# Kernel tuning notes

Measured on AMD Instinct MI355X. Metric: run time of the kernel, lower is better.

## Reference

```python
import jax, jax.numpy as jnp
import numpy as np

BN_EPS = 1e-3
NUM_HEADS = 4
HEAD_CH = 16  # embed_channels // num_heads = 64 // 4


def _conv_bn(x, w, g, b, rm, rv, pad):
    # Conv2d (no bias) followed by eval-mode BatchNorm2d, activation=Identity.
    y = jax.lax.conv_general_dilated(
        x, w, window_strides=(1, 1), padding=[(pad, pad), (pad, pad)],
        dimension_numbers=("NCHW", "OIHW", "NCHW"))
    s = g * jax.lax.rsqrt(rv + BN_EPS)
    return y * s[None, :, None, None] + (b - rm * s)[None, :, None, None]


def setup_inputs() -> dict:
    key = jax.random.key(0)
    ks = jax.random.split(key, 16)
    B, Cin, H, W = 8, 128, 160, 160
    N, Cg, Ce, Co = 80, 512, 64, 128
    x = jax.random.normal(ks[0], (B, Cin, H, W), jnp.float32)
    guide = jax.random.normal(ks[1], (B, N, Cg), jnp.float32)
    # embed_conv (1x1) + BN params
    w_embed = jax.random.normal(ks[2], (Ce, Cin, 1, 1), jnp.float32) * 0.05
    g1 = jnp.ones((Ce,), jnp.float32)
    b1 = jnp.zeros((Ce,), jnp.float32)
    rm1 = jax.random.normal(ks[3], (Ce,), jnp.float32) * 0.1
    rv1 = jax.random.uniform(ks[4], (Ce,), jnp.float32) + 0.5
    # guide_fc
    Wg = jax.random.normal(ks[5], (Ce, Cg), jnp.float32) * 0.02
    bg = jnp.zeros((Ce,), jnp.float32)
    # per-head bias
    attn_bias = jnp.zeros((NUM_HEADS,), jnp.float32)
    # project_conv (3x3) + BN params
    w_proj = jax.random.normal(ks[6], (Co, Cin, 3, 3), jnp.float32) * 0.02
    g2 = jnp.ones((Co,), jnp.float32)
    b2 = jnp.zeros((Co,), jnp.float32)
    rm2 = jax.random.normal(ks[7], (Co,), jnp.float32) * 0.1
    rv2 = jax.random.uniform(ks[8], (Co,), jnp.float32) + 0.5
    return {"x": x, "guide": guide, "w_embed": w_embed, "g1": g1, "b1": b1,
            "rm1": rm1, "rv1": rv1, "Wg": Wg, "bg": bg, "attn_bias": attn_bias,
            "w_proj": w_proj, "g2": g2, "b2": b2, "rm2": rm2, "rv2": rv2}


def reference(x, guide, w_embed, g1, b1, rm1, rv1, Wg, bg, attn_bias,
              w_proj, g2, b2, rm2, rv2):
    B, _, H, W = x.shape
    nh, hc = NUM_HEADS, HEAD_CH
    # guide_fc -> [B, N, nh, hc]
    g = (jnp.einsum("bnc,ec->bne", guide, Wg) + bg).reshape(B, -1, nh, hc)
    # embed_conv (1x1, BN, no act) -> [B, nh, hc, H, W]
    e = _conv_bn(x, w_embed, g1, b1, rm1, rv1, 0).reshape(B, nh, hc, H, W)
    # attn: dot over head channels, max over N guides, scale, bias, sigmoid
    aw = jnp.einsum("bmchw,bnmc->bmhwn", e, g)  # [B, nh, H, W, N]
    aw = jnp.max(aw, axis=-1) * (1.0 / np.sqrt(hc)) + attn_bias[None, :, None, None]
    aw = jax.nn.sigmoid(aw)  # scale == 1.0 (with_scale=False)
    # project_conv (3x3, BN, no act), gate per-head, merge heads
    xp = _conv_bn(x, w_proj, g2, b2, rm2, rv2, 1).reshape(B, nh, -1, H, W)
    return (xp * aw[:, :, None]).reshape(B, -1, H, W)
```

## Files before the change

### kernel.cpp

```cpp
#include <hip/hip_runtime.h>
#include <hip/hip_bf16.h>
#include <stdint.h>


typedef __attribute__((ext_vector_type(8))) short short8;
typedef __attribute__((ext_vector_type(4))) float f32x4;

#define PCH2 ((size_t)8 * 162 * 176 * 32)

__device__ __forceinline__ unsigned short f2bf(float f) {
  unsigned int u = __float_as_uint(f);
  u += 0x7fff + ((u >> 16) & 1);
  return (unsigned short)(u >> 16);
}

__device__ __forceinline__ short8 zero8() {
  short8 z = {0,0,0,0,0,0,0,0};
  return z;
}

__global__ __launch_bounds__(192) void k_prep_x(const float* __restrict__ x,
                                                unsigned short* __restrict__ P2) {
  int b = blockIdx.x / 162, hp = blockIdx.x % 162;
  int wp = threadIdx.x;
  if (wp >= 176) return;
  size_t pix = (((size_t)b * 162 + hp) * 176 + wp) * 32;
  bool interior = (hp >= 1) && (hp <= 160) && (wp >= 8) && (wp < 168);
  if (!interior) {
#pragma unroll
    for (int cs = 0; cs < 4; ++cs)
#pragma unroll
      for (int s = 0; s < 4; ++s)
        *(short8*)(&P2[(size_t)cs * PCH2 + pix + s * 8]) = zero8();
    return;
  }
  int h = hp - 1, w = wp - 8;
  const float* xb = x + (size_t)b * 128 * 25600 + h * 160 + w;
  for (int cs = 0; cs < 4; ++cs) {
#pragma unroll
    for (int s = 0; s < 4; ++s) {
      short8 v;
#pragma unroll
      for (int j = 0; j < 8; ++j) {
        float f = xb[(size_t)(cs * 32 + s * 8 + j) * 25600];
        v[j] = (short)f2bf(f);
      }
      *(short8*)(&P2[(size_t)cs * PCH2 + pix + s * 8]) = v;
    }
  }
}

__global__ __launch_bounds__(256) void k_prep_misc(
    const float* __restrict__ w_embed, const float* __restrict__ w_proj,
    const float* __restrict__ g2, const float* __restrict__ b2,
    const float* __restrict__ rm2, const float* __restrict__ rv2,
    unsigned short* __restrict__ W1t, unsigned short* __restrict__ Wpt,
    float* __restrict__ s2, float* __restrict__ t2) {
  int idx = blockIdx.x * 256 + threadIdx.x;
  if (idx < 8192) { W1t[idx] = f2bf(w_embed[idx]); return; }
  idx -= 8192;
  if (idx < 147456) {
    int cs = idx / 36864, r = idx - cs * 36864;
    int tap = r >> 12, r2 = r & 4095;
    int co = r2 >> 5, ci5 = r2 & 31;
    int ci = cs * 32 + ci5;
    Wpt[idx] = f2bf(w_proj[(co * 128 + ci) * 9 + tap]);
    return;
  }
  idx -= 147456;
  if (idx < 128) {
    float s = g2[idx] * rsqrtf(rv2[idx] + 1e-3f);
    s2[idx] = s;
    t2[idx] = b2[idx] - rm2[idx] * s;
  }
}

__global__ __launch_bounds__(64) void k_guide(
    const float* __restrict__ guide, const float* __restrict__ Wg,
    const float* __restrict__ bg, const float* __restrict__ g1,
    const float* __restrict__ b1, const float* __restrict__ rm1,
    const float* __restrict__ rv1, unsigned short* __restrict__ Gpad,
    float* __restrict__ Cst) {
  int b = blockIdx.x / 80, n = blockIdx.x % 80;
  __shared__ float gs[512];
  const float* gr = guide + ((size_t)b * 80 + n) * 512;
  for (int i = threadIdx.x; i < 512; i += 64) gs[i] = gr[i];
  __syncthreads();
  int ce = threadIdx.x;
  const float* wr = Wg + (size_t)ce * 512;
  float acc = 0.f;
  for (int k = 0; k < 512; k += 4)
    acc += gs[k] * wr[k] + gs[k + 1] * wr[k + 1] + gs[k + 2] * wr[k + 2] +
           gs[k + 3] * wr[k + 3];
  float raw = acc + bg[ce];
  float s1 = g1[ce] * rsqrtf(rv1[ce] + 1e-3f);
  float t1 = b1[ce] - rm1[ce] * s1;
  int head = ce >> 4, c = ce & 15;
  size_t gp = (((size_t)b * 4 + head) * 80 + n) * 32;
  Gpad[gp + c] = f2bf(raw * s1);
  Gpad[gp + 16 + c] = 0;
  float cp = raw * t1;
  cp += __shfl_xor(cp, 1);
  cp += __shfl_xor(cp, 2);
  cp += __shfl_xor(cp, 4);
  cp += __shfl_xor(cp, 8);
  if (c == 0) Cst[((size_t)b * 4 + head) * 80 + n] = cp;
}

__global__ __launch_bounds__(256, 2) void k_mega(
    const unsigned short* __restrict__ P2, const unsigned short* __restrict__ W1t,
    const unsigned short* __restrict__ Wpt, const unsigned short* __restrict__ Gpad,
    const float* __restrict__ Cst, const float* __restrict__ attn_bias,
    const float* __restrict__ s2, const float* __restrict__ t2,
    float* __restrict__ out) {
  __shared__ unsigned short XA[2][7680];
  __shared__ float AWL[4][2][64];
  int b = blockIdx.x & 7, r2b = blockIdx.x >> 3;
  int ht = r2b / 5, wt = r2b % 5;
  int h0 = ht * 4, w0 = wt * 32;
  int tid = threadIdx.x, lane = tid & 63, wv = tid >> 6;
  int l15 = lane & 15, l4 = lane >> 4;
  int mh = wv >> 1, nh = wv & 1;

  size_t aoff[4];
  bool aval[4];
#pragma unroll
  for (int i = 0; i < 4; ++i) {
    int c = i * 256 + tid;
    aval[i] = (c < 960);
    int cc = aval[i] ? c : 0;
    int row = cc / 160, rem = cc - row * 160;
    int px = rem >> 2, sp = rem & 3;
    int s = sp ^ ((px >> 1) & 3);
    aoff[i] = (((size_t)b * 162 + h0 + row) * 176 + (w0 + 7 + px)) * 32 + s * 8;
  }
  int abase[2][3];
#pragma unroll
  for (int wh = 0; wh < 2; ++wh)
#pragma unroll
    for (int kx = 0; kx < 3; ++kx) {
      int px = wh * 16 + l15 + kx;
      abase[wh][kx] = px * 4 + (l4 ^ ((px >> 1) & 3));
    }
  int bfo = (nh * 64 + l15 * 1 * 16 % 16, 0);
  int bco = (nh * 64 + l15) * 0;
  int boff[4];
#pragma unroll
  for (int nt = 0; nt < 4; ++nt) boff[nt] = (nh * 64 + nt * 16 + l15) * 32 + l4 * 8;

  f32x4 acc[4][4], accE[4][2];
#pragma unroll
  for (int j = 0; j < 4; ++j) {
#pragma unroll
    for (int nt = 0; nt < 4; ++nt) acc[j][nt] = (f32x4){0.f, 0.f, 0.f, 0.f};
#pragma unroll
    for (int ne = 0; ne < 2; ++ne) accE[j][ne] = (f32x4){0.f, 0.f, 0.f, 0.f};
  }

  short8 areg[4];
#pragma unroll
  for (int i = 0; i < 4; ++i)
    if (aval[i]) areg[i] = *(const short8*)(P2 + aoff[i]);
#pragma unroll
  for (int i = 0; i < 4; ++i)
    if (aval[i]) *(short8*)(&XA[0][(i * 256 + tid) * 8]) = areg[i];

  short8 Bbuf[3][4];
#pragma unroll
  for (int nt = 0; nt < 4; ++nt) {
    Bbuf[0][nt] = *(const short8*)(Wpt + boff[nt]);
    Bbuf[1][nt] = *(const short8*)(Wpt + 4096 + boff[nt]);
  }
  __syncthreads();

#pragma unroll
  for (int cs = 0; cs < 4; ++cs) {
    if (cs < 3) {
#pragma unroll
      for (int i = 0; i < 4; ++i)
        if (aval[i]) areg[i] = *(const short8*)(P2 + (size_t)(cs + 1) * PCH2 + aoff[i]);
    }
#pragma unroll
    for (int tap = 0; tap < 9; ++tap) {
      const int t = cs * 9 + tap;
      if (t + 2 < 36) {
#pragma unroll
        for (int nt = 0; nt < 4; ++nt)
          Bbuf[(t + 2) % 3][nt] =
              *(const short8*)(Wpt + (size_t)(t + 2) * 4096 + boff[nt]);
      }
      int ky = tap / 3, kx = tap - ky * 3;
      short8 A[4];
#pragma unroll
      for (int j = 0; j < 4; ++j) {
        int rr = mh * 2 + (j >> 1) + ky;
        A[j] = *(const short8*)(&XA[cs & 1][(rr * 160 + abase[j & 1][kx]) * 8]);
      }
      if (tap == 4) {
        short8 BE[2];
#pragma unroll
        for (int ne = 0; ne < 2; ++ne)
          BE[ne] = *(const short8*)(W1t + (nh * 32 + ne * 16 + l15) * 128 +
                                    cs * 32 + l4 * 8);
#pragma unroll
        for (int j = 0; j < 4; ++j)
#pragma unroll
          for (int ne = 0; ne < 2; ++ne)
            accE[j][ne] = __builtin_amdgcn_mfma_f32_16x16x32_bf16(
                A[j], BE[ne], accE[j][ne], 0, 0, 0);
      }
#pragma unroll
      for (int j = 0; j < 4; ++j)
#pragma unroll
        for (int nt = 0; nt < 4; ++nt)
          acc[j][nt] = __builtin_amdgcn_mfma_f32_16x16x32_bf16(
              A[j], Bbuf[t % 3][nt], acc[j][nt], 0, 0, 0);
    }
    if (cs < 3) {
#pragma unroll
      for (int i = 0; i < 4; ++i)
        if (aval[i]) *(short8*)(&XA[(cs + 1) & 1][(i * 256 + tid) * 8]) = areg[i];
      __syncthreads();
    }
  }
  __syncthreads();

  unsigned short* E = &XA[0][0];
#pragma unroll
  for (int j = 0; j < 4; ++j)
#pragma unroll
    for (int ne = 0; ne < 2; ++ne)
#pragma unroll
      for (int r = 0; r < 4; ++r) {
        int pxl = mh * 64 + (j >> 1) * 32 + (j & 1) * 16 + l4 * 4 + r;
        int ce = nh * 32 + ne * 16 + l15;
        int slot = (ce >> 3) ^ (pxl & 7);
        E[pxl * 64 + slot * 8 + (ce & 7)] = f2bf(accE[j][ne][r]);
      }
  __syncthreads();

  const f32x4 zf = (f32x4){0.f, 0.f, 0.f, 0.f};
#pragma unroll
  for (int hh = 0; hh < 2; ++hh) {
    int head = nh * 2 + hh;
    short8 Ga[5];
    f32x4 cst[5];
#pragma unroll
    for (int m5 = 0; m5 < 5; ++m5) {
      Ga[m5] = *(const short8*)(Gpad + (((size_t)b * 4 + head) * 80 + m5 * 16 + l15) * 32 + l4 * 8);
      cst[m5] = *(const f32x4*)(Cst + ((size_t)b * 4 + head) * 80 + m5 * 16 + l4 * 4);
    }
    float bias = attn_bias[head];
#pragma unroll
    for (int nt = 0; nt < 4; ++nt) {
      int pxl = mh * 64 + nt * 16 + l15;
      int rslot = (head * 2 + (l4 & 1)) ^ (pxl & 7);
      short8 Bf = *(const short8*)(E + pxl * 64 + rslot * 8);
      float mx = -3.0e38f;
#pragma unroll
      for (int m5 = 0; m5 < 5; ++m5) {
        f32x4 s = __builtin_amdgcn_mfma_f32_16x16x32_bf16(Ga[m5], Bf, zf, 0, 0, 0);
#pragma unroll
        for (int r = 0; r < 4; ++r) mx = fmaxf(mx, s[r] + cst[m5][r]);
      }
      mx = fmaxf(mx, __shfl_xor(mx, 16));
      mx = fmaxf(mx, __shfl_xor(mx, 32));
      if (lane < 16) AWL[wv][hh][nt * 16 + lane] = 1.f / (1.f + __expf(-(mx * 0.25f + bias)));
    }
  }

  float s2v[4], t2v[4];
#pragma unroll
  for (int nt = 0; nt < 4; ++nt) {
    int co = nh * 64 + nt * 16 + l15;
    s2v[nt] = s2[co];
    t2v[nt] = t2[co];
  }
#pragma unroll
  for (int j = 0; j < 4; ++j) {
    int h = h0 + mh * 2 + (j >> 1);
    int wbase = w0 + (j & 1) * 16 + l4 * 4;
    int pb = (j >> 1) * 32 + (j & 1) * 16 + l4 * 4;
    f32x4 a0 = *(const f32x4*)(&AWL[wv][0][pb]);
    f32x4 a1 = *(const f32x4*)(&AWL[wv][1][pb]);
#pragma unroll
    for (int nt = 0; nt < 4; ++nt) {
      int co = nh * 64 + nt * 16 + l15;
      f32x4 g = (nt >> 1) ? a1 : a0;
      f32x4 o;
#pragma unroll
      for (int r = 0; r < 4; ++r) o[r] = (acc[j][nt][r] * s2v[nt] + t2v[nt]) * g[r];
      *(f32x4*)(out + (size_t)(b * 128 + co) * 25600 + h * 160 + wbase) = o;
    }
  }
}

extern "C" void kernel_launch(void* const* d_in, const int* in_sizes, int n_in,
                              void* d_out, int out_size, void* d_ws, size_t ws_size,
                              hipStream_t stream) {
  (void)in_sizes; (void)n_in; (void)out_size; (void)ws_size;
  const float* x         = (const float*)d_in[0];
  const float* guide     = (const float*)d_in[1];
  const float* w_embed   = (const float*)d_in[2];
  const float* g1        = (const float*)d_in[3];
  const float* b1        = (const float*)d_in[4];
  const float* rm1       = (const float*)d_in[5];
  const float* rv1       = (const float*)d_in[6];
  const float* Wg        = (const float*)d_in[7];
  const float* bg        = (const float*)d_in[8];
  const float* attn_bias = (const float*)d_in[9];
  const float* w_proj    = (const float*)d_in[10];
  const float* g2        = (const float*)d_in[11];
  const float* b2        = (const float*)d_in[12];
  const float* rm2       = (const float*)d_in[13];
  const float* rv2       = (const float*)d_in[14];
  float* out = (float*)d_out;

  char* ws = (char*)d_ws;
  unsigned short* P2   = (unsigned short*)(ws);
  unsigned short* W1t  = (unsigned short*)(ws + 58392576);
  unsigned short* Wpt  = (unsigned short*)(ws + 58408960);
  unsigned short* Gpad = (unsigned short*)(ws + 58703872);
  float* Cst           = (float*)(ws + 58867712);
  float* s2            = (float*)(ws + 58877952);
  float* t2            = (float*)(ws + 58878464);

  k_prep_x<<<8 * 162, 192, 0, stream>>>(x, P2);
  k_prep_misc<<<609, 256, 0, stream>>>(w_embed, w_proj, g2, b2, rm2, rv2, W1t, Wpt, s2, t2);
  k_guide<<<640, 64, 0, stream>>>(guide, Wg, bg, g1, b1, rm1, rv1, Gpad, Cst);
  k_mega<<<1600, 256, 0, stream>>>(P2, W1t, Wpt, Gpad, Cst, attn_bias, s2, t2, out);
}
```

Before: 162.3 us.

## Stage conv weights through double-buffered LDS and split prep_x across more threads

The 3x3 conv weight tile for each tap is now loaded cooperatively into a swizzled, double-buffered LDS array instead of each wave holding a 3-deep register ring of per-lane global loads. This frees registers, so occupancy is raised to 3 blocks per SM. In exchange, a __syncthreads is added after every tap. Separately, k_prep_x now assigns one thread per (pixel, 8-channel slot) rather than one thread per pixel, which gives more parallelism and smaller per-thread work.

```diff
diff --git a/kernel.cpp b/kernel.cpp
--- a/kernel.cpp
+++ b/kernel.cpp
@@ -19,34 +19,30 @@
   return z;
 }
 
-__global__ __launch_bounds__(192) void k_prep_x(const float* __restrict__ x,
+__global__ __launch_bounds__(256) void k_prep_x(const float* __restrict__ x,
                                                 unsigned short* __restrict__ P2) {
-  int b = blockIdx.x / 162, hp = blockIdx.x % 162;
-  int wp = threadIdx.x;
-  if (wp >= 176) return;
-  size_t pix = (((size_t)b * 162 + hp) * 176 + wp) * 32;
+  int b = blockIdx.x / 446, blk = blockIdx.x % 446;
+  int px = blk * 64 + (threadIdx.x >> 2), s = threadIdx.x & 3;
+  if (px >= 28512) return;
+  int hp = px / 176, wp = px - hp * 176;
+  size_t pbase = (((size_t)b * 162 + hp) * 176 + wp) * 32 + s * 8;
   bool interior = (hp >= 1) && (hp <= 160) && (wp >= 8) && (wp < 168);
   if (!interior) {
 #pragma unroll
     for (int cs = 0; cs < 4; ++cs)
-#pragma unroll
-      for (int s = 0; s < 4; ++s)
-        *(short8*)(&P2[(size_t)cs * PCH2 + pix + s * 8]) = zero8();
+      *(short8*)(&P2[(size_t)cs * PCH2 + pbase]) = zero8();
     return;
   }
-  int h = hp - 1, w = wp - 8;
-  const float* xb = x + (size_t)b * 128 * 25600 + h * 160 + w;
+  const float* xb = x + (size_t)b * 128 * 25600 + (hp - 1) * 160 + (wp - 8);
+#pragma unroll
   for (int cs = 0; cs < 4; ++cs) {
-#pragma unroll
-    for (int s = 0; s < 4; ++s) {
-      short8 v;
-#pragma unroll
-      for (int j = 0; j < 8; ++j) {
-        float f = xb[(size_t)(cs * 32 + s * 8 + j) * 25600];
-        v[j] = (short)f2bf(f);
-      }
-      *(short8*)(&P2[(size_t)cs * PCH2 + pix + s * 8]) = v;
-    }
+    short8 v;
+#pragma unroll
+    for (int j = 0; j < 8; ++j) {
+      float f = xb[(size_t)(cs * 32 + s * 8 + j) * 25600];
+      v[j] = (short)f2bf(f);
+    }
+    *(short8*)(&P2[(size_t)cs * PCH2 + pbase]) = v;
   }
 }
 
@@ -107,13 +103,14 @@
   if (c == 0) Cst[((size_t)b * 4 + head) * 80 + n] = cp;
 }
 
-__global__ __launch_bounds__(256, 2) void k_mega(
+__global__ __launch_bounds__(256, 3) void k_mega(
     const unsigned short* __restrict__ P2, const unsigned short* __restrict__ W1t,
     const unsigned short* __restrict__ Wpt, const unsigned short* __restrict__ Gpad,
     const float* __restrict__ Cst, const float* __restrict__ attn_bias,
     const float* __restrict__ s2, const float* __restrict__ t2,
     float* __restrict__ out) {
   __shared__ unsigned short XA[2][7680];
+  __shared__ unsigned short XB[2][4096];
   __shared__ float AWL[4][2][64];
   int b = blockIdx.x & 7, r2b = blockIdx.x >> 3;
   int ht = r2b / 5, wt = r2b % 5;
@@ -134,6 +131,13 @@
     int s = sp ^ ((px >> 1) & 3);
     aoff[i] = (((size_t)b * 162 + h0 + row) * 176 + (w0 + 7 + px)) * 32 + s * 8;
   }
+  int boff[2];
+#pragma unroll
+  for (int i = 0; i < 2; ++i) {
+    int c = i * 256 + tid;
+    int co = c >> 2, sp = c & 3;
+    boff[i] = co * 32 + (sp ^ ((co >> 1) & 3)) * 8;
+  }
   int abase[2][3];
 #pragma unroll
   for (int wh = 0; wh < 2; ++wh)
@@ -142,11 +146,12 @@
       int px = wh * 16 + l15 + kx;
       abase[wh][kx] = px * 4 + (l4 ^ ((px >> 1) & 3));
     }
-  int bfo = (nh * 64 + l15 * 1 * 16 % 16, 0);
-  int bco = (nh * 64 + l15) * 0;
-  int boff[4];
-#pragma unroll
-  for (int nt = 0; nt < 4; ++nt) boff[nt] = (nh * 64 + nt * 16 + l15) * 32 + l4 * 8;
+  int bchunk[4];
+#pragma unroll
+  for (int nt = 0; nt < 4; ++nt) {
+    int co = nh * 64 + nt * 16 + l15;
+    bchunk[nt] = co * 4 + (l4 ^ ((co >> 1) & 3));
+  }
 
   f32x4 acc[4][4], accE[4][2];
 #pragma unroll
@@ -157,20 +162,17 @@
     for (int ne = 0; ne < 2; ++ne) accE[j][ne] = (f32x4){0.f, 0.f, 0.f, 0.f};
   }
 
-  short8 areg[4];
+  short8 areg[4], breg[2];
 #pragma unroll
   for (int i = 0; i < 4; ++i)
     if (aval[i]) areg[i] = *(const short8*)(P2 + aoff[i]);
 #pragma unroll
+  for (int i = 0; i < 2; ++i) breg[i] = *(const short8*)(Wpt + boff[i]);
+#pragma unroll
   for (int i = 0; i < 4; ++i)
     if (aval[i]) *(short8*)(&XA[0][(i * 256 + tid) * 8]) = areg[i];
-
-  short8 Bbuf[3][4];
-#pragma unroll
-  for (int nt = 0; nt < 4; ++nt) {
-    Bbuf[0][nt] = *(const short8*)(Wpt + boff[nt]);
-    Bbuf[1][nt] = *(const short8*)(Wpt + 4096 + boff[nt]);
-  }
+#pragma unroll
+  for (int i = 0; i < 2; ++i) *(short8*)(&XB[0][(i * 256 + tid) * 8]) = breg[i];
   __syncthreads();
 
 #pragma unroll
@@ -183,19 +185,21 @@
 #pragma unroll
     for (int tap = 0; tap < 9; ++tap) {
       const int t = cs * 9 + tap;
-      if (t + 2 < 36) {
-#pragma unroll
-        for (int nt = 0; nt < 4; ++nt)
-          Bbuf[(t + 2) % 3][nt] =
-              *(const short8*)(Wpt + (size_t)(t + 2) * 4096 + boff[nt]);
+      if (t < 35) {
+#pragma unroll
+        for (int i = 0; i < 2; ++i)
+          breg[i] = *(const short8*)(Wpt + (size_t)(t + 1) * 4096 + boff[i]);
       }
       int ky = tap / 3, kx = tap - ky * 3;
-      short8 A[4];
+      short8 A[4], Bf[4];
 #pragma unroll
       for (int j = 0; j < 4; ++j) {
         int rr = mh * 2 + (j >> 1) + ky;
         A[j] = *(const short8*)(&XA[cs & 1][(rr * 160 + abase[j & 1][kx]) * 8]);
       }
+#pragma unroll
+      for (int nt = 0; nt < 4; ++nt)
+        Bf[nt] = *(const short8*)(&XB[t & 1][bchunk[nt] * 8]);
       if (tap == 4) {
         short8 BE[2];
 #pragma unroll
@@ -214,13 +218,18 @@
 #pragma unroll
         for (int nt = 0; nt < 4; ++nt)
           acc[j][nt] = __builtin_amdgcn_mfma_f32_16x16x32_bf16(
-              A[j], Bbuf[t % 3][nt], acc[j][nt], 0, 0, 0);
-    }
-    if (cs < 3) {
-#pragma unroll
-      for (int i = 0; i < 4; ++i)
-        if (aval[i]) *(short8*)(&XA[(cs + 1) & 1][(i * 256 + tid) * 8]) = areg[i];
-      __syncthreads();
+              A[j], Bf[nt], acc[j][nt], 0, 0, 0);
+      if (t < 35) {
+#pragma unroll
+        for (int i = 0; i < 2; ++i)
+          *(short8*)(&XB[(t + 1) & 1][(i * 256 + tid) * 8]) = breg[i];
+      }
+      if (tap == 8 && cs < 3) {
+#pragma unroll
+        for (int i = 0; i < 4; ++i)
+          if (aval[i]) *(short8*)(&XA[(cs + 1) & 1][(i * 256 + tid) * 8]) = areg[i];
+      }
+      if (t < 35) __syncthreads();
     }
   }
   __syncthreads();
@@ -325,7 +334,7 @@
   float* s2            = (float*)(ws + 58877952);
   float* t2            = (float*)(ws + 58878464);
 
-  k_prep_x<<<8 * 162, 192, 0, stream>>>(x, P2);
+  k_prep_x<<<8 * 446, 256, 0, stream>>>(x, P2);
   k_prep_misc<<<609, 256, 0, stream>>>(w_embed, w_proj, g2, b2, rm2, rv2, W1t, Wpt, s2, t2);
   k_guide<<<640, 64, 0, stream>>>(guide, Wg, bg, g1, b1, rm1, rv1, Gpad, Cst);
   k_mega<<<1600, 256, 0, stream>>>(P2, W1t, Wpt, Gpad, Cst, attn_bias, s2, t2, out);
```

Measured after the change: 204.5 us. +26.0%, slower.

## Split output channels across two blocks and coalesce prep_x writes via LDS

Applied to the files above, without the earlier changes.

The fused conv kernel now launches twice as many blocks, each computing half of the output channels (64) and two of the four attention heads. This halves the per-thread accumulators and B fragments, so occupancy can rise to 3 blocks per SIMD group. The cost is that each input tile is loaded and staged into LDS twice. The x-prep kernel is restructured to flatten padded pixels over 256-thread blocks and transpose through swizzled shared memory, so the bf16 packed writes are coalesced.

```diff
diff --git a/kernel.cpp b/kernel.cpp
--- a/kernel.cpp
+++ b/kernel.cpp
@@ -14,38 +14,42 @@
   return (unsigned short)(u >> 16);
 }
 
-__device__ __forceinline__ short8 zero8() {
-  short8 z = {0,0,0,0,0,0,0,0};
-  return z;
-}
-
-__global__ __launch_bounds__(192) void k_prep_x(const float* __restrict__ x,
+__global__ __launch_bounds__(256) void k_prep_x(const float* __restrict__ x,
                                                 unsigned short* __restrict__ P2) {
-  int b = blockIdx.x / 162, hp = blockIdx.x % 162;
-  int wp = threadIdx.x;
-  if (wp >= 176) return;
-  size_t pix = (((size_t)b * 162 + hp) * 176 + wp) * 32;
-  bool interior = (hp >= 1) && (hp <= 160) && (wp >= 8) && (wp < 168);
-  if (!interior) {
-#pragma unroll
-    for (int cs = 0; cs < 4; ++cs)
-#pragma unroll
-      for (int s = 0; s < 4; ++s)
-        *(short8*)(&P2[(size_t)cs * PCH2 + pix + s * 8]) = zero8();
-    return;
-  }
-  int h = hp - 1, w = wp - 8;
-  const float* xb = x + (size_t)b * 128 * 25600 + h * 160 + w;
+  __shared__ unsigned short T[8192];
+  int b = blockIdx.x / 112, blk = blockIdx.x % 112;
+  int tid = threadIdx.x;
+  int px = blk * 256 + tid;
+  int hp = px / 176, wp = px - hp * 176;
+  bool interior = (px < 28512) && (hp >= 1) && (hp <= 160) && (wp >= 8) && (wp < 168);
+  const float* xb = x + (size_t)b * 128 * 25600 + (hp - 1) * 160 + (wp - 8);
+  int q = tid >> 2, os = tid & 3;
+
   for (int cs = 0; cs < 4; ++cs) {
+    short8 v[4];
 #pragma unroll
     for (int s = 0; s < 4; ++s) {
-      short8 v;
 #pragma unroll
       for (int j = 0; j < 8; ++j) {
-        float f = xb[(size_t)(cs * 32 + s * 8 + j) * 25600];
-        v[j] = (short)f2bf(f);
-      }
-      *(short8*)(&P2[(size_t)cs * PCH2 + pix + s * 8]) = v;
+        float f = interior ? xb[(size_t)(cs * 32 + s * 8 + j) * 25600] : 0.f;
+        v[s][j] = (short)f2bf(f);
+      }
+    }
+    if (cs) __syncthreads();
+#pragma unroll
+    for (int s = 0; s < 4; ++s)
+      *(short8*)(&T[(tid * 4 + (s ^ (tid & 3))) * 8]) = v[s];
+    __syncthreads();
+#pragma unroll
+    for (int ph = 0; ph < 4; ++ph) {
+      int lpx = ph * 64 + q;
+      int opx = blk * 256 + lpx;
+      if (opx < 28512) {
+        int ohp = opx / 176, owp = opx - ohp * 176;
+        size_t obase = (((size_t)b * 162 + ohp) * 176 + owp) * 32 + os * 8;
+        short8 w = *(const short8*)(&T[(lpx * 4 + (os ^ (lpx & 3))) * 8]);
+        *(short8*)(&P2[(size_t)cs * PCH2 + obase]) = w;
+      }
     }
   }
 }
@@ -107,16 +111,18 @@
   if (c == 0) Cst[((size_t)b * 4 + head) * 80 + n] = cp;
 }
 
-__global__ __launch_bounds__(256, 2) void k_mega(
+__global__ __launch_bounds__(256, 3) void k_mega(
     const unsigned short* __restrict__ P2, const unsigned short* __restrict__ W1t,
     const unsigned short* __restrict__ Wpt, const unsigned short* __restrict__ Gpad,
     const float* __restrict__ Cst, const float* __restrict__ attn_bias,
     const float* __restrict__ s2, const float* __restrict__ t2,
     float* __restrict__ out) {
   __shared__ unsigned short XA[2][7680];
-  __shared__ float AWL[4][2][64];
-  int b = blockIdx.x & 7, r2b = blockIdx.x >> 3;
-  int ht = r2b / 5, wt = r2b % 5;
+  int b = blockIdx.x & 7;
+  int r = blockIdx.x >> 3;
+  int blkN = r & 1;
+  int tile = r >> 1;
+  int ht = tile / 5, wt = tile - ht * 5;
   int h0 = ht * 4, w0 = wt * 32;
   int tid = threadIdx.x, lane = tid & 63, wv = tid >> 6;
   int l15 = lane & 15, l4 = lane >> 4;
@@ -142,35 +148,32 @@
       int px = wh * 16 + l15 + kx;
       abase[wh][kx] = px * 4 + (l4 ^ ((px >> 1) & 3));
     }
-  int bfo = (nh * 64 + l15 * 1 * 16 % 16, 0);
-  int bco = (nh * 64 + l15) * 0;
-  int boff[4];
-#pragma unroll
-  for (int nt = 0; nt < 4; ++nt) boff[nt] = (nh * 64 + nt * 16 + l15) * 32 + l4 * 8;
-
-  f32x4 acc[4][4], accE[4][2];
+  int boff2[2];
+#pragma unroll
+  for (int nt = 0; nt < 2; ++nt)
+    boff2[nt] = (blkN * 64 + nh * 32 + nt * 16 + l15) * 32 + l4 * 8;
+
+  f32x4 acc[4][2], accE[4];
 #pragma unroll
   for (int j = 0; j < 4; ++j) {
-#pragma unroll
-    for (int nt = 0; nt < 4; ++nt) acc[j][nt] = (f32x4){0.f, 0.f, 0.f, 0.f};
-#pragma unroll
-    for (int ne = 0; ne < 2; ++ne) accE[j][ne] = (f32x4){0.f, 0.f, 0.f, 0.f};
+    acc[j][0] = (f32x4){0.f, 0.f, 0.f, 0.f};
+    acc[j][1] = (f32x4){0.f, 0.f, 0.f, 0.f};
+    accE[j]   = (f32x4){0.f, 0.f, 0.f, 0.f};
   }
 
   short8 areg[4];
 #pragma unroll
   for (int i = 0; i < 4; ++i)
     if (aval[i]) areg[i] = *(const short8*)(P2 + aoff[i]);
+  short8 Bb[3][2];
+#pragma unroll
+  for (int nt = 0; nt < 2; ++nt) {
+    Bb[0][nt] = *(const short8*)(Wpt + boff2[nt]);
+    Bb[1][nt] = *(const short8*)(Wpt + 4096 + boff2[nt]);
+  }
 #pragma unroll
   for (int i = 0; i < 4; ++i)
     if (aval[i]) *(short8*)(&XA[0][(i * 256 + tid) * 8]) = areg[i];
-
-  short8 Bbuf[3][4];
-#pragma unroll
-  for (int nt = 0; nt < 4; ++nt) {
-    Bbuf[0][nt] = *(const short8*)(Wpt + boff[nt]);
-    Bbuf[1][nt] = *(const short8*)(Wpt + 4096 + boff[nt]);
-  }
   __syncthreads();
 
 #pragma unroll
@@ -185,9 +188,9 @@
       const int t = cs * 9 + tap;
       if (t + 2 < 36) {
 #pragma unroll
-        for (int nt = 0; nt < 4; ++nt)
-          Bbuf[(t + 2) % 3][nt] =
-              *(const short8*)(Wpt + (size_t)(t + 2) * 4096 + boff[nt]);
+        for (int nt = 0; nt < 2; ++nt)
+          Bb[(t + 2) % 3][nt] =
+              *(const short8*)(Wpt + (size_t)(t + 2) * 4096 + boff2[nt]);
       }
       int ky = tap / 3, kx = tap - ky * 3;
       short8 A[4];
@@ -197,24 +200,18 @@
         A[j] = *(const short8*)(&XA[cs & 1][(rr * 160 + abase[j & 1][kx]) * 8]);
       }
       if (tap == 4) {
-        short8 BE[2];
-#pragma unroll
-        for (int ne = 0; ne < 2; ++ne)
-          BE[ne] = *(const short8*)(W1t + (nh * 32 + ne * 16 + l15) * 128 +
-                                    cs * 32 + l4 * 8);
+        short8 BE = *(const short8*)(W1t + (blkN * 32 + nh * 16 + l15) * 128 +
+                                     cs * 32 + l4 * 8);
 #pragma unroll
         for (int j = 0; j < 4; ++j)
-#pragma unroll
-          for (int ne = 0; ne < 2; ++ne)
-            accE[j][ne] = __builtin_amdgcn_mfma_f32_16x16x32_bf16(
-                A[j], BE[ne], accE[j][ne], 0, 0, 0);
+          accE[j] = __builtin_amdgcn_mfma_f32_16x16x32_bf16(A[j], BE, accE[j], 0, 0, 0);
       }
 #pragma unroll
       for (int j = 0; j < 4; ++j)
 #pragma unroll
-        for (int nt = 0; nt < 4; ++nt)
+        for (int nt = 0; nt < 2; ++nt)
           acc[j][nt] = __builtin_amdgcn_mfma_f32_16x16x32_bf16(
-              A[j], Bbuf[t % 3][nt], acc[j][nt], 0, 0, 0);
+              A[j], Bb[t % 3][nt], acc[j][nt], 0, 0, 0);
     }
     if (cs < 3) {
 #pragma unroll
@@ -225,54 +222,48 @@
   }
   __syncthreads();
 
-  unsigned short* E = &XA[0][0];
+  unsigned short* Eb = &XA[0][0];
+  float* AWLf = (float*)(&XA[0][0] + 4096);
 #pragma unroll
   for (int j = 0; j < 4; ++j)
 #pragma unroll
-    for (int ne = 0; ne < 2; ++ne)
-#pragma unroll
-      for (int r = 0; r < 4; ++r) {
-        int pxl = mh * 64 + (j >> 1) * 32 + (j & 1) * 16 + l4 * 4 + r;
-        int ce = nh * 32 + ne * 16 + l15;
-        int slot = (ce >> 3) ^ (pxl & 7);
-        E[pxl * 64 + slot * 8 + (ce & 7)] = f2bf(accE[j][ne][r]);
-      }
-  __syncthreads();
+    for (int rr = 0; rr < 4; ++rr) {
+      int pxl = (j >> 1) * 32 + (j & 1) * 16 + l4 * 4 + rr;
+      int chunk = (l15 >> 3) ^ (pxl & 1);
+      Eb[wv * 1024 + pxl * 16 + chunk * 8 + (l15 & 7)] = f2bf(accE[j][rr]);
+    }
 
   const f32x4 zf = (f32x4){0.f, 0.f, 0.f, 0.f};
-#pragma unroll
-  for (int hh = 0; hh < 2; ++hh) {
-    int head = nh * 2 + hh;
-    short8 Ga[5];
-    f32x4 cst[5];
+  int head = blkN * 2 + nh;
+  short8 Ga[5];
+  f32x4 cst[5];
+#pragma unroll
+  for (int m5 = 0; m5 < 5; ++m5) {
+    Ga[m5] = *(const short8*)(Gpad + (((size_t)b * 4 + head) * 80 + m5 * 16 + l15) * 32 + l4 * 8);
+    cst[m5] = *(const f32x4*)(Cst + ((size_t)b * 4 + head) * 80 + m5 * 16 + l4 * 4);
+  }
+  float bias = attn_bias[head];
+#pragma unroll
+  for (int nt = 0; nt < 4; ++nt) {
+    int pxl = nt * 16 + l15;
+    int chr = (l4 & 1) ^ (pxl & 1);
+    short8 Bf = *(const short8*)(&Eb[wv * 1024 + pxl * 16 + chr * 8]);
+    float mx = -3.0e38f;
 #pragma unroll
     for (int m5 = 0; m5 < 5; ++m5) {
-      Ga[m5] = *(const short8*)(Gpad + (((size_t)b * 4 + head) * 80 + m5 * 16 + l15) * 32 + l4 * 8);
-      cst[m5] = *(const f32x4*)(Cst + ((size_t)b * 4 + head) * 80 + m5 * 16 + l4 * 4);
-    }
-    float bias = attn_bias[head];
-#pragma unroll
-    for (int nt = 0; nt < 4; ++nt) {
-      int pxl = mh * 64 + nt * 16 + l15;
-      int rslot = (head * 2 + (l4 & 1)) ^ (pxl & 7);
-      short8 Bf = *(const short8*)(E + pxl * 64 + rslot * 8);
-      float mx = -3.0e38f;
-#pragma unroll
-      for (int m5 = 0; m5 < 5; ++m5) {
-        f32x4 s = __builtin_amdgcn_mfma_f32_16x16x32_bf16(Ga[m5], Bf, zf, 0, 0, 0);
-#pragma unroll
-        for (int r = 0; r < 4; ++r) mx = fmaxf(mx, s[r] + cst[m5][r]);
-      }
-      mx = fmaxf(mx, __shfl_xor(mx, 16));
-      mx = fmaxf(mx, __shfl_xor(mx, 32));
-      if (lane < 16) AWL[wv][hh][nt * 16 + lane] = 1.f / (1.f + __expf(-(mx * 0.25f + bias)));
-    }
-  }
-
-  float s2v[4], t2v[4];
-#pragma unroll
-  for (int nt = 0; nt < 4; ++nt) {
-    int co = nh * 64 + nt * 16 + l15;
+      f32x4 s = __builtin_amdgcn_mfma_f32_16x16x32_bf16(Ga[m5], Bf, zf, 0, 0, 0);
+#pragma unroll
+      for (int rr = 0; rr < 4; ++rr) mx = fmaxf(mx, s[rr] + cst[m5][rr]);
+    }
+    mx = fmaxf(mx, __shfl_xor(mx, 16));
+    mx = fmaxf(mx, __shfl_xor(mx, 32));
+    if (lane < 16) AWLf[wv * 64 + nt * 16 + lane] = 1.f / (1.f + __expf(-(mx * 0.25f + bias)));
+  }
+
+  float s2v[2], t2v[2];
+#pragma unroll
+  for (int nt = 0; nt < 2; ++nt) {
+    int co = blkN * 64 + nh * 32 + nt * 16 + l15;
     s2v[nt] = s2[co];
     t2v[nt] = t2[co];
   }
@@ -281,15 +272,13 @@
     int h = h0 + mh * 2 + (j >> 1);
     int wbase = w0 + (j & 1) * 16 + l4 * 4;
     int pb = (j >> 1) * 32 + (j & 1) * 16 + l4 * 4;
-    f32x4 a0 = *(const f32x4*)(&AWL[wv][0][pb]);
-    f32x4 a1 = *(const f32x4*)(&AWL[wv][1][pb]);
-#pragma unroll
-    for (int nt = 0; nt < 4; ++nt) {
-      int co = nh * 64 + nt * 16 + l15;
-      f32x4 g = (nt >> 1) ? a1 : a0;
+    f32x4 a0 = *(const f32x4*)(&AWLf[wv * 64 + pb]);
+#pragma unroll
+    for (int nt = 0; nt < 2; ++nt) {
+      int co = blkN * 64 + nh * 32 + nt * 16 + l15;
       f32x4 o;
 #pragma unroll
-      for (int r = 0; r < 4; ++r) o[r] = (acc[j][nt][r] * s2v[nt] + t2v[nt]) * g[r];
+      for (int rr = 0; rr < 4; ++rr) o[rr] = (acc[j][nt][rr] * s2v[nt] + t2v[nt]) * a0[rr];
       *(f32x4*)(out + (size_t)(b * 128 + co) * 25600 + h * 160 + wbase) = o;
     }
   }
@@ -325,8 +314,8 @@
   float* s2            = (float*)(ws + 58877952);
   float* t2            = (float*)(ws + 58878464);
 
-  k_prep_x<<<8 * 162, 192, 0, stream>>>(x, P2);
+  k_prep_x<<<8 * 112, 256, 0, stream>>>(x, P2);
   k_prep_misc<<<609, 256, 0, stream>>>(w_embed, w_proj, g2, b2, rm2, rv2, W1t, Wpt, s2, t2);
   k_guide<<<640, 64, 0, stream>>>(guide, Wg, bg, g1, b1, rm1, rv1, Gpad, Cst);
-  k_mega<<<1600, 256, 0, stream>>>(P2, W1t, Wpt, Gpad, Cst, attn_bias, s2, t2, out);
-}
+  k_mega<<<3200, 256, 0, stream>>>(P2, W1t, Wpt, Gpad, Cst, attn_bias, s2, t2, out);
+}
```

Result: faster. 145.8 us (-10.2%).
